# Performance work log

Hardware: AMD Instinct MI355X
Metric: run time of the kernel (lower is better)

Reference implementation:

```python
import jax, jax.numpy as jnp
import numpy as np

B, T, D, E = 2, 8192, 256, 8
TWO_D = 2 * D
N = B * T
CAP = N // E            # expert-choice capacity per expert
PRIME_DELAYS = (1, 2, 3, 5)
LOCAL_ITERS = 8
BASE_LR = 0.5
LR_DECAY = 0.85


def setup_inputs() -> dict:
    key = jax.random.key(0)
    ks = jax.random.split(key, 6)
    x_stream = jax.random.normal(ks[0], (B, T, D, 2), jnp.float32)
    phase = jax.random.uniform(ks[1], (D,), jnp.float32) * (2.0 * np.float32(np.pi))
    cos_p = jnp.cos(phase)
    sin_p = jnp.sin(phase)
    delay_gains = jax.random.normal(ks[2], (len(PRIME_DELAYS), D, 2), jnp.float32) * 0.02
    gate_w = jax.random.normal(ks[3], (TWO_D, E), jnp.float32) * np.float32(1.0 / np.sqrt(TWO_D))
    expert_w = jax.random.normal(ks[4], (E, TWO_D, TWO_D), jnp.float32) * np.float32(1.0 / np.sqrt(TWO_D))
    act_bias = jax.random.normal(ks[5], (D, 2), jnp.float32) * 0.01
    return {"x_stream": x_stream, "delay_gains": delay_gains, "cos_p": cos_p,
            "sin_p": sin_p, "gate_w": gate_w, "expert_w": expert_w, "act_bias": act_bias}


def _phase_targets(x, cos_p, sin_p):
    # target[:,1:] = phase-rotated x[:,:-1]; target[:,0] = x[:,0]
    pr, pi = x[:, :-1, :, 0], x[:, :-1, :, 1]
    rot = jnp.stack([pr * cos_p - pi * sin_p, pr * sin_p + pi * cos_p], axis=-1)
    return jnp.concatenate([x[:, :1], rot], axis=1)


def _apply_delays(x, gains):
    # x_eff[:, tau:] += complex_mul(x[:, :-tau], gain[tau])  (reads original x)
    xe = x
    for i, tau in enumerate(PRIME_DELAYS):
        gr, gi = gains[i, :, 0], gains[i, :, 1]
        dr, di = x[:, :-tau, :, 0], x[:, :-tau, :, 1]
        upd = jnp.stack([dr * gr - di * gi, dr * gi + di * gr], axis=-1)
        xe = xe.at[:, tau:].add(upd)
    return xe


def _moe(x_eff, gate_w, expert_w):
    # Expert-choice MoE: softmax gate per token, each expert picks top-CAP tokens.
    xf = x_eff.reshape(N, TWO_D)
    scores = jax.nn.softmax(xf @ gate_w, axis=-1)          # [N, E]
    vals, idx = jax.lax.top_k(scores.T, CAP)               # [E, CAP]
    xg = xf[idx]                                           # [E, CAP, 2D]
    yo = jnp.einsum('ecd,edf->ecf', xg, expert_w)          # [E, CAP, 2D]
    flat_idx = idx.reshape(-1)
    pred = jnp.zeros((N, TWO_D), xf.dtype).at[flat_idx].add((vals[..., None] * yo).reshape(-1, TWO_D))
    counts = jnp.zeros((N,), xf.dtype).at[flat_idx].add(1.0)
    return pred.reshape(B, T, D, 2), counts


def _normalize_activate(pred, counts, act_bias):
    denom = jnp.maximum(counts, 1.0).reshape(B, T, 1, 1)
    return jnp.tanh(pred / denom + act_bias)


def reference(x_stream, delay_gains, cos_p, sin_p, gate_w, expert_w, act_bias):
    x = x_stream.astype(jnp.float32)
    x_target_frozen = _phase_targets(x, cos_p, sin_p)

    # ---- no-grad fixed-point inner loop (local_iters == min_iters == 8 => fixed 8 iters) ----
    x_states = x
    lr = BASE_LR
    pred = counts = None
    for _ in range(LOCAL_ITERS):
        x_eff = _apply_delays(x_states, delay_gains)
        pred, counts = _moe(x_eff, gate_w, expert_w)
        residual = x_target_frozen - pred
        x_states = x_states + lr * jnp.clip(residual, -10.0, 10.0)
        lr = lr * LR_DECAY
    x_states = jax.lax.stop_gradient(_normalize_activate(pred, counts, act_bias))
    x_target_ng = jax.lax.stop_gradient(x_target_frozen)

    # ---- differentiable tail ----
    x_target_grad = _phase_targets(x, cos_p, sin_p)
    x_eff_grad = _apply_delays(x_states, delay_gains)
    pred_grad, _ = _moe(x_eff_grad, gate_w, expert_w)
    out = x_states + BASE_LR * (x_target_grad - pred_grad)
    res_norm = jnp.linalg.norm(x_target_ng - pred_grad, axis=-1).mean()
    return out.astype(x_stream.dtype), res_norm
```

## Files before the change

kernel.cpp:

```cpp
#include <hip/hip_runtime.h>

#define T_    8192
#define D_    256
#define E_    8
#define TWOD  512
#define NTOK  16384
#define CAP_  2048
#define NQ    (NTOK * 128)

__global__ __launch_bounds__(256) void init_kernel(const float4* __restrict__ x,
    const float* __restrict__ cosp, const float* __restrict__ sinp,
    float4* __restrict__ xt, float4* __restrict__ xs)
{
  int q = blockIdx.x * 256 + threadIdx.x;
  int n = q >> 7, dq = q & 127, t = n & (T_ - 1);
  float4 v = x[q];
  xs[q] = v;
  float4 g;
  if (t == 0) {
    g = v;
  } else {
    float4 p = x[q - 128];
    int d0 = dq * 2;
    float c0 = cosp[d0], s0 = sinp[d0], c1 = cosp[d0 + 1], s1 = sinp[d0 + 1];
    g.x = p.x * c0 - p.y * s0;
    g.y = p.x * s0 + p.y * c0;
    g.z = p.z * c1 - p.w * s1;
    g.w = p.z * s1 + p.w * c1;
  }
  xt[q] = g;
}

__global__ __launch_bounds__(256) void delays_gate_kernel(const float4* __restrict__ xs,
    const float* __restrict__ gains, const float* __restrict__ gw,
    float4* __restrict__ xe, float* __restrict__ scoresT)
{
  int q = blockIdx.x * 256 + threadIdx.x;
  int n = q >> 7, dq = q & 127, t = n & (T_ - 1);
  float4 v = xs[q];
  const int taus[4] = {1, 2, 3, 5};
  int d0 = dq * 2;
  #pragma unroll
  for (int i = 0; i < 4; i++) {
    int tau = taus[i];
    if (t >= tau) {
      float4 p = xs[q - tau * 128];
      float gr0 = gains[(i * D_ + d0) * 2 + 0], gi0 = gains[(i * D_ + d0) * 2 + 1];
      float gr1 = gains[(i * D_ + d0 + 1) * 2 + 0], gi1 = gains[(i * D_ + d0 + 1) * 2 + 1];
      v.x += p.x * gr0 - p.y * gi0;
      v.y += p.x * gi0 + p.y * gr0;
      v.z += p.z * gr1 - p.w * gi1;
      v.w += p.z * gi1 + p.w * gr1;
    }
  }
  xe[q] = v;

  float p8[8] = {0, 0, 0, 0, 0, 0, 0, 0};
  const float4* gw4 = (const float4*)gw;
  float av[4] = {v.x, v.y, v.z, v.w};
  #pragma unroll
  for (int j = 0; j < 4; j++) {
    float4 w0 = gw4[(dq * 4 + j) * 2];
    float4 w1 = gw4[(dq * 4 + j) * 2 + 1];
    float a = av[j];
    p8[0] = fmaf(a, w0.x, p8[0]);
    p8[1] = fmaf(a, w0.y, p8[1]);
    p8[2] = fmaf(a, w0.z, p8[2]);
    p8[3] = fmaf(a, w0.w, p8[3]);
    p8[4] = fmaf(a, w1.x, p8[4]);
    p8[5] = fmaf(a, w1.y, p8[5]);
    p8[6] = fmaf(a, w1.z, p8[6]);
    p8[7] = fmaf(a, w1.w, p8[7]);
  }
  #pragma unroll
  for (int off = 32; off > 0; off >>= 1)
    #pragma unroll
    for (int e = 0; e < 8; e++) p8[e] += __shfl_down(p8[e], off);
  __shared__ float red[4][8];
  int wv = threadIdx.x >> 6;
  if ((threadIdx.x & 63) == 0)
    #pragma unroll
    for (int e = 0; e < 8; e++) red[wv][e] = p8[e];
  __syncthreads();
  if (threadIdx.x < 2) {
    int tok = blockIdx.x * 2 + threadIdx.x;
    float pe[8], m = -1e30f;
    #pragma unroll
    for (int e = 0; e < 8; e++) {
      pe[e] = red[threadIdx.x * 2][e] + red[threadIdx.x * 2 + 1][e];
      m = fmaxf(m, pe[e]);
    }
    float ssum = 0.f;
    #pragma unroll
    for (int e = 0; e < 8; e++) { pe[e] = expf(pe[e] - m); ssum += pe[e]; }
    float inv = 1.0f / ssum;
    #pragma unroll
    for (int e = 0; e < 8; e++) scoresT[e * NTOK + tok] = pe[e] * inv;
  }
}

__global__ __launch_bounds__(1024) void select_kernel(const float* __restrict__ scoresT,
    int* __restrict__ idxl, int* __restrict__ slot_of)
{
  int e = blockIdx.x;
  const float* s = scoresT + (size_t)e * NTOK;
  int tid = threadIdx.x;
  int lane = tid & 63, wv = tid >> 6;

  float4 f[4];
  #pragma unroll
  for (int j = 0; j < 4; j++) f[j] = ((const float4*)s)[tid + 1024 * j];
  unsigned uv[16];
  #pragma unroll
  for (int j = 0; j < 4; j++) {
    uv[j * 4 + 0] = __float_as_uint(f[j].x);
    uv[j * 4 + 1] = __float_as_uint(f[j].y);
    uv[j * 4 + 2] = __float_as_uint(f[j].z);
    uv[j * 4 + 3] = __float_as_uint(f[j].w);
  }

  __shared__ int hist[16][257];
  __shared__ int histsum[256];
  __shared__ int sfx[2][256];
  __shared__ int wsum[16], wpre[16];
  __shared__ int shB, shK, shTot, scnt;

  unsigned prefix = 0;
  int k = CAP_;
  for (int p = 0; p < 4; ++p) {
    int shift = 24 - 8 * p;
    for (int b = tid; b < 16 * 257; b += 1024) ((int*)hist)[b] = 0;
    __syncthreads();
    #pragma unroll
    for (int r = 0; r < 16; r++) {
      unsigned u = uv[r];
      bool match = (p == 0) || ((u >> (shift + 8)) == prefix);
      if (match) atomicAdd(&hist[wv][(u >> shift) & 255], 1);
    }
    __syncthreads();
    if (tid < 256) {
      int tsum = 0;
      #pragma unroll
      for (int w = 0; w < 16; w++) tsum += hist[w][tid];
      histsum[tid] = tsum;
      sfx[0][tid] = tsum;
    }
    __syncthreads();
    int cur = 0;
    #pragma unroll
    for (int d = 1; d < 256; d <<= 1) {
      if (tid < 256)
        sfx[cur ^ 1][tid] = sfx[cur][tid] + ((tid + d < 256) ? sfx[cur][tid + d] : 0);
      __syncthreads();
      cur ^= 1;
    }
    if (tid < 256) {
      int sv = sfx[cur][tid];
      int snext = (tid < 255) ? sfx[cur][tid + 1] : 0;
      if (sv >= k && snext < k) { shB = tid; shK = k - snext; }
    }
    __syncthreads();
    prefix = (prefix << 8) | (unsigned)shB;
    k = shK;
    __syncthreads();
  }
  unsigned thr = prefix;
  int kk = k;

  if (tid == 0) scnt = 0;
  __syncthreads();
  int jb = 0;
  #pragma unroll
  for (int j = 0; j < 4; j++) {
    int eqf[4], c = 0;
    #pragma unroll
    for (int cc = 0; cc < 4; cc++) {
      eqf[cc] = (uv[j * 4 + cc] == thr) ? 1 : 0;
      c += eqf[cc];
    }
    int sc = c;
    #pragma unroll
    for (int d = 1; d < 64; d <<= 1) {
      int tt = __shfl_up(sc, d);
      if (lane >= d) sc += tt;
    }
    if (lane == 63) wsum[wv] = sc;
    __syncthreads();
    if (tid == 0) {
      int a = 0;
      #pragma unroll
      for (int w = 0; w < 16; w++) { int t2 = wsum[w]; wpre[w] = a; a += t2; }
      shTot = a;
    }
    __syncthreads();
    int excl = wpre[wv] + (sc - c);
    int local = 0;
    int sov[4];
    #pragma unroll
    for (int cc = 0; cc < 4; cc++) {
      unsigned u = uv[j * 4 + cc];
      int n = 4 * tid + 4096 * j + cc;
      bool take = (u > thr) || (eqf[cc] && (jb + excl + local) < kk);
      local += eqf[cc];
      unsigned long long msk = __ballot(take);
      int cntw = __popcll(msk);
      int base = 0;
      if (lane == 0 && cntw) base = atomicAdd(&scnt, cntw);
      base = __shfl(base, 0);
      int slot = base + __popcll(msk & ((1ull << lane) - 1ull));
      int sv = -1;
      if (take) {
        idxl[e * CAP_ + slot] = n;
        sv = slot;
      }
      sov[cc] = sv;
    }
    int4 so;
    so.x = sov[0]; so.y = sov[1]; so.z = sov[2]; so.w = sov[3];
    ((int4*)(slot_of + (size_t)e * NTOK))[tid + 1024 * j] = so;
    jb += shTot;
    __syncthreads();
  }
}

#define GM 128
#define GN 128
#define GKK 16
__device__ __forceinline__ float comp4(const float4 v, int u) {
  return u == 0 ? v.x : u == 1 ? v.y : u == 2 ? v.z : v.w;
}
__device__ __forceinline__ void gl_lds16(const void* g, void* l) {
  __builtin_amdgcn_global_load_lds(
      (const __attribute__((address_space(1))) unsigned int*)g,
      (__attribute__((address_space(3))) unsigned int*)l, 16, 0, 0);
}
__global__ __launch_bounds__(256) void gemm_kernel(const float* __restrict__ xe,
    const float* __restrict__ ew, const int* __restrict__ idxl, float* __restrict__ yo)
{
  int bid0 = blockIdx.x;
  int bid = (bid0 & 7) * 64 + (bid0 >> 3);
  int e = bid >> 6, rem = bid & 63, mt = rem >> 2, nt = rem & 3;
  __shared__ float4 AB[2 * 1024];
  int tid = threadIdx.x;
  int tx = tid & 15, ty = tid >> 4;
  const float* We = ew + (size_t)e * TWOD * TWOD + nt * GN;

  const float* aptr0[2];
  const float* bptr0[2];
  #pragma unroll
  for (int l = 0; l < 2; l++) {
    int slot = l * 256 + tid;
    int row = slot >> 2, kqs = slot & 3;
    int kq = kqs ^ ((row >> 3) & 3);
    int tok = idxl[e * CAP_ + mt * GM + row];
    aptr0[l] = xe + (size_t)tok * TWOD + kq * 4;
    int kkk = slot >> 5, cc = slot & 31;
    bptr0[l] = We + (size_t)kkk * TWOD + cc * 4;
  }
  int wbase = tid & 192;

  auto stage = [&](int buf, int kb) {
    float4* dA = AB + buf * 1024 + wbase;
    float4* dB = dA + 512;
    #pragma unroll
    for (int l = 0; l < 2; l++) {
      gl_lds16(aptr0[l] + kb, (void*)(dA + l * 256));
      gl_lds16(bptr0[l] + (size_t)kb * TWOD, (void*)(dB + l * 256));
    }
  };

  stage(0, 0);
  __syncthreads();

  float acc[8][8] = {};
  int cur = 0;

  for (int kb = GKK; kb <= TWOD; kb += GKK) {
    if (kb < TWOD) stage(cur ^ 1, kb);
    const float4* As4 = AB + cur * 1024;
    const float4* Bs4 = As4 + 512;
    #pragma unroll
    for (int k4 = 0; k4 < GKK; k4 += 4) {
      int kq = k4 >> 2;
      float4 a4[8], b4[8];
      #pragma unroll
      for (int i = 0; i < 8; i++) a4[i] = As4[(ty * 8 + i) * 4 + (kq ^ (ty & 3))];
      #pragma unroll
      for (int u = 0; u < 4; u++) {
        b4[2 * u]     = Bs4[(k4 + u) * 32 + tx];
        b4[2 * u + 1] = Bs4[(k4 + u) * 32 + 16 + tx];
      }
      #pragma unroll
      for (int u = 0; u < 4; u++) {
        float av[8], bv[8];
        #pragma unroll
        for (int i = 0; i < 8; i++) av[i] = comp4(a4[i], u);
        bv[0] = b4[2*u].x; bv[1] = b4[2*u].y; bv[2] = b4[2*u].z; bv[3] = b4[2*u].w;
        bv[4] = b4[2*u+1].x; bv[5] = b4[2*u+1].y; bv[6] = b4[2*u+1].z; bv[7] = b4[2*u+1].w;
        #pragma unroll
        for (int i = 0; i < 8; i++)
          #pragma unroll
          for (int jj = 0; jj < 8; jj++)
            acc[i][jj] = fmaf(av[i], bv[jj], acc[i][jj]);
      }
    }
    __syncthreads();
    cur ^= 1;
  }

  #pragma unroll
  for (int i = 0; i < 8; i++) {
    float* dst = yo + (size_t)(e * CAP_ + mt * GM + ty * 8 + i) * TWOD + nt * GN + tx * 4;
    float4 o0 = {acc[i][0], acc[i][1], acc[i][2], acc[i][3]};
    float4 o1 = {acc[i][4], acc[i][5], acc[i][6], acc[i][7]};
    *(float4*)dst = o0;
    *(float4*)(dst + 64) = o1;
  }
}

__global__ __launch_bounds__(256) void combine_update_kernel(const float4* __restrict__ yo,
    const float* __restrict__ scoresT, const int* __restrict__ slot_of,
    const float4* __restrict__ xt, float4* __restrict__ xs,
    float4* __restrict__ pred, int* __restrict__ counts, float lr, int write_pred)
{
  int q = blockIdx.x * 256 + threadIdx.x;
  int n = q >> 7, dq = q & 127;
  float4 p = {0, 0, 0, 0};
  int cnt = 0;
  #pragma unroll
  for (int e = 0; e < E_; e++) {
    int sl = slot_of[e * NTOK + n];
    if (sl >= 0) {
      float val = scoresT[e * NTOK + n];
      float4 y = yo[(size_t)(e * CAP_ + sl) * 128 + dq];
      p.x = fmaf(val, y.x, p.x);
      p.y = fmaf(val, y.y, p.y);
      p.z = fmaf(val, y.z, p.z);
      p.w = fmaf(val, y.w, p.w);
      cnt++;
    }
  }
  float4 t = xt[q], s = xs[q];
  s.x += lr * fminf(fmaxf(t.x - p.x, -10.f), 10.f);
  s.y += lr * fminf(fmaxf(t.y - p.y, -10.f), 10.f);
  s.z += lr * fminf(fmaxf(t.z - p.z, -10.f), 10.f);
  s.w += lr * fminf(fmaxf(t.w - p.w, -10.f), 10.f);
  xs[q] = s;
  if (write_pred) {
    pred[q] = p;
    if (dq == 0) counts[n] = cnt;
  }
}

__global__ __launch_bounds__(256) void combine_final_kernel(const float4* __restrict__ yo,
    const float* __restrict__ scoresT, const int* __restrict__ slot_of,
    const float4* __restrict__ xt, const float4* __restrict__ xs,
    float4* __restrict__ out, float* __restrict__ racc)
{
  int q = blockIdx.x * 256 + threadIdx.x;
  int n = q >> 7, dq = q & 127;
  float4 p = {0, 0, 0, 0};
  #pragma unroll
  for (int e = 0; e < E_; e++) {
    int sl = slot_of[e * NTOK + n];
    if (sl >= 0) {
      float val = scoresT[e * NTOK + n];
      float4 y = yo[(size_t)(e * CAP_ + sl) * 128 + dq];
      p.x = fmaf(val, y.x, p.x);
      p.y = fmaf(val, y.y, p.y);
      p.z = fmaf(val, y.z, p.z);
      p.w = fmaf(val, y.w, p.w);
    }
  }
  float4 t = xt[q], s = xs[q];
  float dr0 = t.x - p.x, di0 = t.y - p.y, dr1 = t.z - p.z, di1 = t.w - p.w;
  float4 o = {s.x + 0.5f * dr0, s.y + 0.5f * di0, s.z + 0.5f * dr1, s.w + 0.5f * di1};
  out[q] = o;
  float lsum = sqrtf(dr0 * dr0 + di0 * di0) + sqrtf(dr1 * dr1 + di1 * di1);
  __shared__ float red[256];
  red[threadIdx.x] = lsum;
  __syncthreads();
  for (int off = 128; off > 0; off >>= 1) {
    if (threadIdx.x < off) red[threadIdx.x] += red[threadIdx.x + off];
    __syncthreads();
  }
  if (threadIdx.x == 0) atomicAdd(racc, red[0]);
}

__global__ __launch_bounds__(256) void activate_kernel(const float4* __restrict__ pred,
    const int* __restrict__ counts, const float4* __restrict__ bias, float4* __restrict__ xs)
{
  int q = blockIdx.x * 256 + threadIdx.x;
  int n = q >> 7;
  float denom = fmaxf((float)counts[n], 1.0f);
  float4 p = pred[q];
  float4 b = bias[q & 127];
  float4 r;
  r.x = tanhf(p.x / denom + b.x);
  r.y = tanhf(p.y / denom + b.y);
  r.z = tanhf(p.z / denom + b.z);
  r.w = tanhf(p.w / denom + b.w);
  xs[q] = r;
}

__global__ void finish_kernel(const float* __restrict__ racc, float* __restrict__ dst)
{
  if (threadIdx.x == 0) dst[0] = racc[0] / 4194304.0f;
}

extern "C" void kernel_launch(void* const* d_in, const int* in_sizes, int n_in,
                              void* d_out, int out_size, void* d_ws, size_t ws_size,
                              hipStream_t stream)
{
  const float* x     = (const float*)d_in[0];
  const float* gains = (const float*)d_in[1];
  const float* cosp  = (const float*)d_in[2];
  const float* sinp  = (const float*)d_in[3];
  const float* gw    = (const float*)d_in[4];
  const float* ew    = (const float*)d_in[5];
  const float* bias  = (const float*)d_in[6];
  float* out = (float*)d_out;

  char* w = (char*)d_ws;
  size_t off = 0;
  auto alloc = [&](size_t bytes) -> void* {
    void* p = w + off;
    off += (bytes + 255) & ~(size_t)255;
    return p;
  };
  float* xt      = (float*)alloc((size_t)NTOK * TWOD * 4);
  float* xs      = (float*)alloc((size_t)NTOK * TWOD * 4);
  float* xe      = (float*)alloc((size_t)NTOK * TWOD * 4);
  float* pred    = (float*)alloc((size_t)NTOK * TWOD * 4);
  float* yo      = (float*)alloc((size_t)E_ * CAP_ * TWOD * 4);
  float* scoresT = (float*)alloc((size_t)E_ * NTOK * 4);
  int*   idxl    = (int*)  alloc((size_t)E_ * CAP_ * 4);
  int*   slot_of = (int*)  alloc((size_t)E_ * NTOK * 4);
  int*   counts  = (int*)  alloc((size_t)NTOK * 4);
  float* racc    = (float*)alloc(256);

  const int eb = NQ / 256;

  init_kernel<<<eb, 256, 0, stream>>>((const float4*)x, cosp, sinp, (float4*)xt, (float4*)xs);

  double lr = 0.5;
  for (int it = 0; it < 9; ++it) {
    if (it == 8)
      activate_kernel<<<eb, 256, 0, stream>>>((const float4*)pred, counts,
                                              (const float4*)bias, (float4*)xs);
    delays_gate_kernel<<<eb, 256, 0, stream>>>((const float4*)xs, gains, gw,
                                               (float4*)xe, scoresT);
    select_kernel<<<E_, 1024, 0, stream>>>(scoresT, idxl, slot_of);
    gemm_kernel<<<512, 256, 0, stream>>>(xe, ew, idxl, yo);
    if (it < 8) {
      combine_update_kernel<<<eb, 256, 0, stream>>>((const float4*)yo, scoresT, slot_of,
          (const float4*)xt, (float4*)xs, (float4*)pred, counts, (float)lr, it == 7 ? 1 : 0);
      lr *= 0.85;
    } else {
      hipMemsetAsync(racc, 0, 4, stream);
      combine_final_kernel<<<eb, 256, 0, stream>>>((const float4*)yo, scoresT, slot_of,
          (const float4*)xt, (const float4*)xs, (float4*)out, racc);
    }
  }
  finish_kernel<<<1, 64, 0, stream>>>(racc, out + (size_t)NTOK * TWOD);
}
```

Measured before the change: 1.961 ms.

## Fuse combine/update and activation into delay-gate kernel with ping-pong buffers

Removes the separate combine_update and activate kernels by recomputing the expert-combine gather and state update inside the delay+gate kernel, including for the four delayed neighbour tokens. State and score buffers are double-buffered so each iteration reads the previous state and scores while writing new ones. This saves a full pass over the state tensor and the pred/counts round-trip per iteration. In exchange, the gather work (up to 8 expert reads per token) is repeated about five times per output element because of the delay taps.

Measured after the change: 2.192 ms. 11.7% more time.

```diff
diff --git a/kernel.cpp b/kernel.cpp
--- a/kernel.cpp
+++ b/kernel.cpp
@@ -31,33 +31,90 @@
   xt[q] = g;
 }
 
-__global__ __launch_bounds__(256) void delays_gate_kernel(const float4* __restrict__ xs,
-    const float* __restrict__ gains, const float* __restrict__ gw,
-    float4* __restrict__ xe, float* __restrict__ scoresT)
+__device__ __forceinline__ float4 gather_pred(const float* __restrict__ sc_old,
+    const int* __restrict__ slot_of, const float4* __restrict__ yo,
+    int m, int dq, int* cnt_out)
+{
+  float4 p = {0, 0, 0, 0};
+  int cnt = 0;
+  #pragma unroll
+  for (int e = 0; e < E_; e++) {
+    int sl = slot_of[e * NTOK + m];
+    if (sl >= 0) {
+      float val = sc_old[e * NTOK + m];
+      float4 y = yo[(size_t)(e * CAP_ + sl) * 128 + dq];
+      p.x = fmaf(val, y.x, p.x);
+      p.y = fmaf(val, y.y, p.y);
+      p.z = fmaf(val, y.z, p.z);
+      p.w = fmaf(val, y.w, p.w);
+      cnt++;
+    }
+  }
+  *cnt_out = cnt;
+  return p;
+}
+
+__device__ __forceinline__ float4 state_of(int mode, const float4* __restrict__ xsrc,
+    const float4* __restrict__ xt, const float4* __restrict__ bias,
+    const float* __restrict__ sc_old, const int* __restrict__ slot_of,
+    const float4* __restrict__ yo, int m, int dq, float lr)
+{
+  int q = m * 128 + dq;
+  if (mode == 0) return xsrc[q];
+  int cnt;
+  float4 p = gather_pred(sc_old, slot_of, yo, m, dq, &cnt);
+  if (mode == 1) {
+    float4 t = xt[q], s = xsrc[q];
+    s.x += lr * fminf(fmaxf(t.x - p.x, -10.f), 10.f);
+    s.y += lr * fminf(fmaxf(t.y - p.y, -10.f), 10.f);
+    s.z += lr * fminf(fmaxf(t.z - p.z, -10.f), 10.f);
+    s.w += lr * fminf(fmaxf(t.w - p.w, -10.f), 10.f);
+    return s;
+  }
+  float denom = fmaxf((float)cnt, 1.0f);
+  float4 b = bias[dq];
+  float4 r;
+  r.x = tanhf(p.x / denom + b.x);
+  r.y = tanhf(p.y / denom + b.y);
+  r.z = tanhf(p.z / denom + b.z);
+  r.w = tanhf(p.w / denom + b.w);
+  return r;
+}
+
+__global__ __launch_bounds__(256) void fused_kernel(const float4* __restrict__ xsrc,
+    float4* __restrict__ xdst, const float* __restrict__ gains,
+    const float* __restrict__ gw, const float* __restrict__ sc_old,
+    float* __restrict__ sc_new, const int* __restrict__ slot_of,
+    const float4* __restrict__ yo, const float4* __restrict__ xt,
+    const float4* __restrict__ bias, float4* __restrict__ xe, float lr, int mode)
 {
   int q = blockIdx.x * 256 + threadIdx.x;
   int n = q >> 7, dq = q & 127, t = n & (T_ - 1);
-  float4 v = xs[q];
+
+  float4 v = state_of(mode, xsrc, xt, bias, sc_old, slot_of, yo, n, dq, lr);
+  if (mode != 0) xdst[q] = v;
+
+  float4 ve = v;
   const int taus[4] = {1, 2, 3, 5};
   int d0 = dq * 2;
   #pragma unroll
   for (int i = 0; i < 4; i++) {
     int tau = taus[i];
     if (t >= tau) {
-      float4 p = xs[q - tau * 128];
+      float4 p = state_of(mode, xsrc, xt, bias, sc_old, slot_of, yo, n - tau, dq, lr);
       float gr0 = gains[(i * D_ + d0) * 2 + 0], gi0 = gains[(i * D_ + d0) * 2 + 1];
       float gr1 = gains[(i * D_ + d0 + 1) * 2 + 0], gi1 = gains[(i * D_ + d0 + 1) * 2 + 1];
-      v.x += p.x * gr0 - p.y * gi0;
-      v.y += p.x * gi0 + p.y * gr0;
-      v.z += p.z * gr1 - p.w * gi1;
-      v.w += p.z * gi1 + p.w * gr1;
-    }
-  }
-  xe[q] = v;
+      ve.x += p.x * gr0 - p.y * gi0;
+      ve.y += p.x * gi0 + p.y * gr0;
+      ve.z += p.z * gr1 - p.w * gi1;
+      ve.w += p.z * gi1 + p.w * gr1;
+    }
+  }
+  xe[q] = ve;
 
   float p8[8] = {0, 0, 0, 0, 0, 0, 0, 0};
   const float4* gw4 = (const float4*)gw;
-  float av[4] = {v.x, v.y, v.z, v.w};
+  float av[4] = {ve.x, ve.y, ve.z, ve.w};
   #pragma unroll
   for (int j = 0; j < 4; j++) {
     float4 w0 = gw4[(dq * 4 + j) * 2];
@@ -95,7 +152,7 @@
     for (int e = 0; e < 8; e++) { pe[e] = expf(pe[e] - m); ssum += pe[e]; }
     float inv = 1.0f / ssum;
     #pragma unroll
-    for (int e = 0; e < 8; e++) scoresT[e * NTOK + tok] = pe[e] * inv;
+    for (int e = 0; e < 8; e++) sc_new[e * NTOK + tok] = pe[e] * inv;
   }
 }
 
@@ -318,40 +375,6 @@
   }
 }
 
-__global__ __launch_bounds__(256) void combine_update_kernel(const float4* __restrict__ yo,
-    const float* __restrict__ scoresT, const int* __restrict__ slot_of,
-    const float4* __restrict__ xt, float4* __restrict__ xs,
-    float4* __restrict__ pred, int* __restrict__ counts, float lr, int write_pred)
-{
-  int q = blockIdx.x * 256 + threadIdx.x;
-  int n = q >> 7, dq = q & 127;
-  float4 p = {0, 0, 0, 0};
-  int cnt = 0;
-  #pragma unroll
-  for (int e = 0; e < E_; e++) {
-    int sl = slot_of[e * NTOK + n];
-    if (sl >= 0) {
-      float val = scoresT[e * NTOK + n];
-      float4 y = yo[(size_t)(e * CAP_ + sl) * 128 + dq];
-      p.x = fmaf(val, y.x, p.x);
-      p.y = fmaf(val, y.y, p.y);
-      p.z = fmaf(val, y.z, p.z);
-      p.w = fmaf(val, y.w, p.w);
-      cnt++;
-    }
-  }
-  float4 t = xt[q], s = xs[q];
-  s.x += lr * fminf(fmaxf(t.x - p.x, -10.f), 10.f);
-  s.y += lr * fminf(fmaxf(t.y - p.y, -10.f), 10.f);
-  s.z += lr * fminf(fmaxf(t.z - p.z, -10.f), 10.f);
-  s.w += lr * fminf(fmaxf(t.w - p.w, -10.f), 10.f);
-  xs[q] = s;
-  if (write_pred) {
-    pred[q] = p;
-    if (dq == 0) counts[n] = cnt;
-  }
-}
-
 __global__ __launch_bounds__(256) void combine_final_kernel(const float4* __restrict__ yo,
     const float* __restrict__ scoresT, const int* __restrict__ slot_of,
     const float4* __restrict__ xt, const float4* __restrict__ xs,
@@ -387,22 +410,6 @@
   if (threadIdx.x == 0) atomicAdd(racc, red[0]);
 }
 
-__global__ __launch_bounds__(256) void activate_kernel(const float4* __restrict__ pred,
-    const int* __restrict__ counts, const float4* __restrict__ bias, float4* __restrict__ xs)
-{
-  int q = blockIdx.x * 256 + threadIdx.x;
-  int n = q >> 7;
-  float denom = fmaxf((float)counts[n], 1.0f);
-  float4 p = pred[q];
-  float4 b = bias[q & 127];
-  float4 r;
-  r.x = tanhf(p.x / denom + b.x);
-  r.y = tanhf(p.y / denom + b.y);
-  r.z = tanhf(p.z / denom + b.z);
-  r.w = tanhf(p.w / denom + b.w);
-  xs[q] = r;
-}
-
 __global__ void finish_kernel(const float* __restrict__ racc, float* __restrict__ dst)
 {
   if (threadIdx.x == 0) dst[0] = racc[0] / 4194304.0f;
@@ -429,38 +436,38 @@
     return p;
   };
   float* xt      = (float*)alloc((size_t)NTOK * TWOD * 4);
-  float* xs      = (float*)alloc((size_t)NTOK * TWOD * 4);
+  float* X0      = (float*)alloc((size_t)NTOK * TWOD * 4);
+  float* X1      = (float*)alloc((size_t)NTOK * TWOD * 4);
   float* xe      = (float*)alloc((size_t)NTOK * TWOD * 4);
-  float* pred    = (float*)alloc((size_t)NTOK * TWOD * 4);
   float* yo      = (float*)alloc((size_t)E_ * CAP_ * TWOD * 4);
-  float* scoresT = (float*)alloc((size_t)E_ * NTOK * 4);
+  float* S0      = (float*)alloc((size_t)E_ * NTOK * 4);
+  float* S1      = (float*)alloc((size_t)E_ * NTOK * 4);
   int*   idxl    = (int*)  alloc((size_t)E_ * CAP_ * 4);
   int*   slot_of = (int*)  alloc((size_t)E_ * NTOK * 4);
-  int*   counts  = (int*)  alloc((size_t)NTOK * 4);
   float* racc    = (float*)alloc(256);
+  float* X[2] = {X0, X1};
+  float* S[2] = {S0, S1};
 
   const int eb = NQ / 256;
 
-  init_kernel<<<eb, 256, 0, stream>>>((const float4*)x, cosp, sinp, (float4*)xt, (float4*)xs);
-
-  double lr = 0.5;
-  for (int it = 0; it < 9; ++it) {
-    if (it == 8)
-      activate_kernel<<<eb, 256, 0, stream>>>((const float4*)pred, counts,
-                                              (const float4*)bias, (float4*)xs);
-    delays_gate_kernel<<<eb, 256, 0, stream>>>((const float4*)xs, gains, gw,
-                                               (float4*)xe, scoresT);
-    select_kernel<<<E_, 1024, 0, stream>>>(scoresT, idxl, slot_of);
+  init_kernel<<<eb, 256, 0, stream>>>((const float4*)x, cosp, sinp, (float4*)xt, (float4*)X0);
+
+  double lrv = 0.5;
+  for (int it = 0; it <= 8; ++it) {
+    int mode = (it == 0) ? 0 : (it == 8) ? 2 : 1;
+    const float* src = (const float*)X[(it == 0) ? 0 : ((it - 1) & 1)];
+    float* dst = X[it & 1];
+    const float* scold = S[(it == 0) ? 1 : ((it - 1) & 1)];
+    float lr = (float)((it >= 1) ? lrv : 0.0);
+    fused_kernel<<<eb, 256, 0, stream>>>((const float4*)src, (float4*)dst, gains, gw,
+        scold, S[it & 1], slot_of, (const float4*)yo, (const float4*)xt,
+        (const float4*)bias, (float4*)xe, lr, mode);
+    if (it >= 1 && it < 8) lrv *= 0.85;
+    select_kernel<<<E_, 1024, 0, stream>>>(S[it & 1], idxl, slot_of);
     gemm_kernel<<<512, 256, 0, stream>>>(xe, ew, idxl, yo);
-    if (it < 8) {
-      combine_update_kernel<<<eb, 256, 0, stream>>>((const float4*)yo, scoresT, slot_of,
-          (const float4*)xt, (float4*)xs, (float4*)pred, counts, (float)lr, it == 7 ? 1 : 0);
-      lr *= 0.85;
-    } else {
-      hipMemsetAsync(racc, 0, 4, stream);
-      combine_final_kernel<<<eb, 256, 0, stream>>>((const float4*)yo, scoresT, slot_of,
-          (const float4*)xt, (const float4*)xs, (float4*)out, racc);
-    }
-  }
+  }
+  hipMemsetAsync(racc, 0, 4, stream);
+  combine_final_kernel<<<eb, 256, 0, stream>>>((const float4*)yo, S[0], slot_of,
+      (const float4*)xt, (const float4*)X0, (float4*)out, racc);
   finish_kernel<<<1, 64, 0, stream>>>(racc, out + (size_t)NTOK * TWOD);
 }
```
